# Kernel optimization log

Hardware: AMD Instinct MI355X
Metric: run time of the kernel (lower is better)

The kernel has to match this reference:

```python
import jax, jax.numpy as jnp
import numpy as np

N, E, D, H, O, G = 50000, 800000, 64, 64, 32, 64


def setup_inputs() -> dict:
    key = jax.random.key(0)
    ks = jax.random.split(key, 12)
    x = jax.random.normal(ks[0], (N, D), dtype=jnp.float32)
    edge_index = jax.random.randint(ks[1], (2, E), 0, N)
    batch = jnp.sort(jax.random.randint(ks[2], (N,), 0, G))

    def glorot(k, fan_in, fan_out):
        s = np.sqrt(6.0 / (fan_in + fan_out)).astype(np.float32)
        return jax.random.uniform(k, (fan_in, fan_out), jnp.float32, -s, s)

    return {
        "x": x,
        "edge_index": edge_index,
        "batch": batch,
        "W1": glorot(ks[3], D, H), "b1": jnp.zeros((H,), jnp.float32),
        "W2": glorot(ks[4], H, H), "b2": jnp.zeros((H,), jnp.float32),
        "W3": glorot(ks[5], H, H), "b3": jnp.zeros((H,), jnp.float32),
        "Wl": glorot(ks[6], H, O), "bl": jnp.zeros((O,), jnp.float32),
    }


def reference(x, edge_index, batch, W1, b1, W2, b2, W3, b3, Wl, bl):
    n = x.shape[0]
    # GCNConv default: add self-loops, symmetric deg^-1/2 normalization
    loop = jnp.arange(n, dtype=edge_index.dtype)
    src = jnp.concatenate([edge_index[0], loop])  # [E+N]
    dst = jnp.concatenate([edge_index[1], loop])
    deg = jax.ops.segment_sum(jnp.ones_like(src, dtype=x.dtype), dst, num_segments=n)
    dis = jax.lax.rsqrt(deg)  # deg >= 1 due to self-loops
    norm = (dis[src] * dis[dst])[:, None]  # [E+N, 1]

    def gcn(h, W, b):
        hw = h @ W                      # [N, H] small GEMM
        msg = hw[src] * norm            # gather + scale: [E+N, H]
        agg = jax.ops.segment_sum(msg, dst, num_segments=n)  # scatter-add
        return agg + b

    h = jax.nn.relu(gcn(x, W1, b1))
    h = jax.nn.relu(gcn(h, W2, b2))
    h = gcn(h, W3, b3)

    # global_mean_pool over graph ids
    counts = jax.ops.segment_sum(jnp.ones((n,), h.dtype), batch, num_segments=G)
    pooled = jax.ops.segment_sum(h, batch, num_segments=G) / counts[:, None]

    # dropout(p=0.5) is identity in eval mode
    return pooled @ Wl + bl
```

## Files before the change

### kernel.cpp

```cpp
#include <hip/hip_runtime.h>

#define HD 64
#define PSUB 16
#define NBLK 256
#define LOG_NBLK 8
#define NBKT 512

__device__ __forceinline__ unsigned short f2bf(float f) {
    union { float f; unsigned u; } v; v.f = f;
    unsigned r = v.u + 0x7FFF + ((v.u >> 16) & 1);
    return (unsigned short)(r >> 16);
}
__device__ __forceinline__ float u2f(unsigned u) {
    union { unsigned u; float f; } v; v.u = u;
    return v.f;
}


__global__ __launch_bounds__(256) void hist1_k(const int* __restrict__ dst,
                                               int* __restrict__ hist, int E, int chunk,
                                               float* __restrict__ partial, int psz)
{
    __shared__ int lh[NBKT];
    int t = threadIdx.x;
    for (int i = t; i < NBKT; i += 256) lh[i] = 0;
    for (int i = blockIdx.x * 256 + t; i < psz; i += gridDim.x * 256)
        partial[i] = 0.f;
    __syncthreads();
    int base = blockIdx.x * chunk;
    int end  = min(base + chunk, E);
    for (int i = base + t; i < end; i += 256)
        atomicAdd(&lh[dst[i] >> 7], 1);
    __syncthreads();
    for (int i = t; i < NBKT; i += 256)
        hist[blockIdx.x * NBKT + i] = lh[i];
}

__global__ __launch_bounds__(256) void scanA_k(const int* __restrict__ hist,
                                               int* __restrict__ tsum)
{
    __shared__ int s[256];
    int t = threadIdx.x;
    int l = blockIdx.x * 256 + t;
    int phys = (l & (NBLK - 1)) * NBKT + (l >> LOG_NBLK);
    s[t] = hist[phys];
    __syncthreads();
    for (int off = 128; off > 0; off >>= 1) {
        if (t < off) s[t] += s[t + off];
        __syncthreads();
    }
    if (t == 0) tsum[blockIdx.x] = s[0];
}

__global__ __launch_bounds__(1024) void scanB_k(int* __restrict__ tsum, int nb,
    const int* __restrict__ batch, int* __restrict__ gstart, int n, int G)
{
    __shared__ int s[1024];
    int t = threadIdx.x;
    int v = (t < nb) ? tsum[t] : 0;
    s[t] = v;
    __syncthreads();
    for (int off = 1; off < 1024; off <<= 1) {
        int u = (t >= off) ? s[t - off] : 0;
        __syncthreads();
        s[t] += u;
        __syncthreads();
    }
    if (t < nb) tsum[t] = s[t] - v;
    if (t <= G) {
        if (t == G) gstart[t] = n;
        else {
            int lo = 0, hi = n;
            while (lo < hi) { int m = (lo + hi) >> 1; if (batch[m] < t) lo = m + 1; else hi = m; }
            gstart[t] = lo;
        }
    }
}

__global__ __launch_bounds__(256) void scanC_k(const int* __restrict__ hist,
                                               const int* __restrict__ tsum,
                                               int* __restrict__ scanned)
{
    __shared__ int s[256];
    int t = threadIdx.x;
    int l = blockIdx.x * 256 + t;
    int phys = (l & (NBLK - 1)) * NBKT + (l >> LOG_NBLK);
    int own = hist[phys];
    s[t] = own;
    __syncthreads();
    for (int off = 1; off < 256; off <<= 1) {
        int u = (t >= off) ? s[t - off] : 0;
        __syncthreads();
        s[t] += u;
        __syncthreads();
    }
    scanned[l] = tsum[blockIdx.x] + s[t] - own;
}

__global__ __launch_bounds__(256) void append_k(const int* __restrict__ src,
    const int* __restrict__ dst, const int* __restrict__ scanned,
    int* __restrict__ pairs, int E, int chunk)
{
    __shared__ int cur[NBKT];
    int t = threadIdx.x;
    int blk = blockIdx.x;
    for (int i = t; i < NBKT; i += 256) cur[i] = scanned[i * NBLK + blk];
    __syncthreads();
    int base = blk * chunk;
    int end  = min(base + chunk, E);
    for (int i = base + t; i < end; i += 256) {
        int s = src[i], d = dst[i];
        int p = atomicAdd(&cur[d >> 7], 1);
        pairs[p] = (s << 7) | (d & 127);
    }
}

__global__ __launch_bounds__(256) void bucket_csr_k(const int* __restrict__ pairs,
    const int* __restrict__ scanned, int* __restrict__ offsets,
    float* __restrict__ dis, int* __restrict__ csr_src, int N, int E)
{
    __shared__ int cnt[128];
    __shared__ int sc[128];
    __shared__ int cur[128];
    int t = threadIdx.x;
    int b = blockIdx.x;
    int nodeBase = b * 128;
    int nNodes = min(128, N - nodeBase);
    int bBase = scanned[b * NBLK];
    int bEnd  = (b + 1 < NBKT) ? scanned[(b + 1) * NBLK] : E;

    if (t < 128) cnt[t] = 0;
    __syncthreads();
    for (int i = bBase + t; i < bEnd; i += 256)
        atomicAdd(&cnt[pairs[i] & 127], 1);
    __syncthreads();
    int myc = (t < 128) ? cnt[t] : 0;
    if (t < 128) sc[t] = myc;
    __syncthreads();
    for (int off = 1; off < 128; off <<= 1) {
        int u = (t < 128 && t >= off) ? sc[t - off] : 0;
        __syncthreads();
        if (t < 128) sc[t] += u;
        __syncthreads();
    }
    if (t < 128) {
        int excl = sc[t] - myc;
        cur[t] = excl;
        if (t < nNodes) {
            offsets[nodeBase + t] = bBase + excl;
            dis[nodeBase + t] = rsqrtf(1.0f + (float)myc);
        }
    }
    if (t == 0 && b == gridDim.x - 1) offsets[N] = E;
    __syncthreads();
    for (int i = bBase + t; i < bEnd; i += 256) {
        int pk = pairs[i];
        int pos = bBase + atomicAdd(&cur[pk & 127], 1);
        csr_src[pos] = ((unsigned)pk) >> 7;
    }
}


__global__ __launch_bounds__(256) void gemm64_k(
    const float* __restrict__ in, const float* __restrict__ W,
    const float* __restrict__ dis, unsigned short* __restrict__ outb, int n)
{
    __shared__ float HsT[HD][68];
    __shared__ float Ws[HD][HD];
    int t = threadIdx.x;
    int rowBase = blockIdx.x * 64;

    for (int i = t; i < HD * HD / 4; i += 256)
        ((float4*)Ws)[i] = ((const float4*)W)[i];

    if (blockIdx.x == 0 && t < 64)
        outb[(size_t)n * HD + t] = 0;

    {
        int k0 = (t & 15) * 4;
        for (int it = 0; it < 4; ++it) {
            int r = (t >> 4) + it * 16;
            int row = rowBase + r;
            float4 v = make_float4(0.f, 0.f, 0.f, 0.f);
            if (row < n)
                v = *(const float4*)&in[(size_t)row * HD + k0];
            HsT[k0 + 0][r] = v.x;
            HsT[k0 + 1][r] = v.y;
            HsT[k0 + 2][r] = v.z;
            HsT[k0 + 3][r] = v.w;
        }
    }
    __syncthreads();

    int c4 = (t & 15) * 4;
    int r4 = (t >> 4) * 4;
    float acc[4][4];
    #pragma unroll
    for (int i = 0; i < 4; ++i)
        #pragma unroll
        for (int j = 0; j < 4; ++j) acc[i][j] = 0.f;

    #pragma unroll 8
    for (int k = 0; k < HD; ++k) {
        float4 a = *(const float4*)&HsT[k][r4];
        float4 b = *(const float4*)&Ws[k][c4];
        acc[0][0] += a.x * b.x; acc[0][1] += a.x * b.y; acc[0][2] += a.x * b.z; acc[0][3] += a.x * b.w;
        acc[1][0] += a.y * b.x; acc[1][1] += a.y * b.y; acc[1][2] += a.y * b.z; acc[1][3] += a.y * b.w;
        acc[2][0] += a.z * b.x; acc[2][1] += a.z * b.y; acc[2][2] += a.z * b.z; acc[2][3] += a.z * b.w;
        acc[3][0] += a.w * b.x; acc[3][1] += a.w * b.y; acc[3][2] += a.w * b.z; acc[3][3] += a.w * b.w;
    }

    #pragma unroll
    for (int i = 0; i < 4; ++i) {
        int row = rowBase + r4 + i;
        if (row < n) {
            float ds = dis[row];
            ushort4 o;
            o.x = f2bf(ds * acc[i][0]); o.y = f2bf(ds * acc[i][1]);
            o.z = f2bf(ds * acc[i][2]); o.w = f2bf(ds * acc[i][3]);
            *(ushort4*)&outb[(size_t)row * HD + c4] = o;
        }
    }
}

__device__ __forceinline__ void gather4(const unsigned short* __restrict__ hwb,
    const int* __restrict__ offsets, const int* __restrict__ csr_src,
    int node, bool act, int n, int sub, int fl,
    float& a0, float& a1, float& a2, float& a3)
{
    int beg = 0, end = 0;
    if (act) { beg = offsets[node]; end = offsets[node + 1]; }
    int deg = end - beg;
    int md = deg;
    md = max(md, __shfl_xor(md, 16, 64));
    md = max(md, __shfl_xor(md, 32, 64));

    int nodeC = act ? node : n;
    uint2 sv = *(const uint2*)(hwb + ((size_t)nodeC << 6) + (fl << 2));
    a0 = u2f(sv.x << 16); a1 = u2f(sv.x & 0xFFFF0000u);
    a2 = u2f(sv.y << 16); a3 = u2f(sv.y & 0xFFFF0000u);

    int base = sub << 4;
    int idxv = (fl < deg) ? csr_src[beg + fl] : n;
    for (int jb = 0; jb < md; jb += 16) {
        int e2 = jb + 16 + fl;
        int nidx = (e2 < deg) ? csr_src[beg + e2] : n;
        {
            uint2 g[8];
            #pragma unroll
            for (int j = 0; j < 8; ++j) {
                int row = __shfl(idxv, base + j, 64);
                g[j] = *(const uint2*)(hwb + ((size_t)row << 6) + (fl << 2));
            }
            #pragma unroll
            for (int j = 0; j < 8; ++j) {
                a0 += u2f(g[j].x << 16); a1 += u2f(g[j].x & 0xFFFF0000u);
                a2 += u2f(g[j].y << 16); a3 += u2f(g[j].y & 0xFFFF0000u);
            }
        }
        if (jb + 8 < md) {
            uint2 g[8];
            #pragma unroll
            for (int j = 0; j < 8; ++j) {
                int row = __shfl(idxv, base + 8 + j, 64);
                g[j] = *(const uint2*)(hwb + ((size_t)row << 6) + (fl << 2));
            }
            #pragma unroll
            for (int j = 0; j < 8; ++j) {
                a0 += u2f(g[j].x << 16); a1 += u2f(g[j].x & 0xFFFF0000u);
                a2 += u2f(g[j].y << 16); a3 += u2f(g[j].y & 0xFFFF0000u);
            }
        }
        idxv = nidx;
    }
}

__global__ __launch_bounds__(256) void agg_gemm_k(
    const unsigned short* __restrict__ hwb, const float* __restrict__ dis,
    const int* __restrict__ offsets, const int* __restrict__ csr_src,
    const float* __restrict__ b_prev, const float* __restrict__ W,
    unsigned short* __restrict__ outb, int n)
{
    __shared__ float As[16][68];
    __shared__ float Ws[HD][HD];
    int t    = threadIdx.x;
    int lane = t & 63;
    int sub  = lane >> 4;
    int fl   = lane & 15;
    int w    = t >> 6;
    int nib  = w * 4 + sub;
    int nodeBase = blockIdx.x * 16;
    int node = nodeBase + nib;
    bool act = node < n;

    for (int i = t; i < HD * HD / 4; i += 256)
        ((float4*)Ws)[i] = ((const float4*)W)[i];

    if (blockIdx.x == 0 && t < 64)
        outb[(size_t)n * HD + t] = 0;

    float a0, a1, a2, a3;
    gather4(hwb, offsets, csr_src, node, act, n, sub, fl, a0, a1, a2, a3);

    float ds = act ? dis[node] : 0.f;
    int c0 = fl << 2;
    float4 bb = *(const float4*)&b_prev[c0];
    float4 v;
    v.x = fmaxf(a0 * ds + bb.x, 0.f);
    v.y = fmaxf(a1 * ds + bb.y, 0.f);
    v.z = fmaxf(a2 * ds + bb.z, 0.f);
    v.w = fmaxf(a3 * ds + bb.w, 0.f);
    *(float4*)&As[nib][c0] = v;
    __syncthreads();

    int r  = t & 15;
    int c4 = (t >> 4) << 2;
    float acc0 = 0.f, acc1 = 0.f, acc2 = 0.f, acc3 = 0.f;
    #pragma unroll 4
    for (int k = 0; k < HD; k += 4) {
        float4 a  = *(const float4*)&As[r][k];
        float4 w0 = *(const float4*)&Ws[k + 0][c4];
        float4 w1 = *(const float4*)&Ws[k + 1][c4];
        float4 w2 = *(const float4*)&Ws[k + 2][c4];
        float4 w3 = *(const float4*)&Ws[k + 3][c4];
        acc0 += a.x * w0.x + a.y * w1.x + a.z * w2.x + a.w * w3.x;
        acc1 += a.x * w0.y + a.y * w1.y + a.z * w2.y + a.w * w3.y;
        acc2 += a.x * w0.z + a.y * w1.z + a.z * w2.z + a.w * w3.z;
        acc3 += a.x * w0.w + a.y * w1.w + a.z * w2.w + a.w * w3.w;
    }
    int orow = nodeBase + r;
    if (orow < n) {
        float d2 = dis[orow];
        ushort4 o;
        o.x = f2bf(d2 * acc0); o.y = f2bf(d2 * acc1);
        o.z = f2bf(d2 * acc2); o.w = f2bf(d2 * acc3);
        *(ushort4*)&outb[(size_t)orow * HD + c4] = o;
    }
}

__global__ __launch_bounds__(256) void agg_pool4_k(const unsigned short* __restrict__ hwb,
    const float* __restrict__ dis, const int* __restrict__ offsets,
    const int* __restrict__ csr_src, const int* __restrict__ batch,
    float* __restrict__ partial, int n)
{
    __shared__ float sh[16][68];
    __shared__ int gids[16];
    __shared__ int allsame;
    int t    = threadIdx.x;
    int lane = t & 63;
    int sub  = lane >> 4;
    int fl   = lane & 15;
    int w    = t >> 6;
    int nib  = w * 4 + sub;
    int node = blockIdx.x * 16 + nib;
    bool act = node < n;

    float a0, a1, a2, a3;
    gather4(hwb, offsets, csr_src, node, act, n, sub, fl, a0, a1, a2, a3);

    float ds = act ? dis[node] : 0.f;
    *(float4*)&sh[nib][fl << 2] = make_float4(a0 * ds, a1 * ds, a2 * ds, a3 * ds);
    if (fl == 0) gids[nib] = act ? batch[node] : -1;
    __syncthreads();

    if (t == 0) {
        int g0 = gids[0];
        int ok = (g0 >= 0);
        #pragma unroll
        for (int r = 1; r < 16; ++r) ok &= (gids[r] == g0);
        allsame = ok;
    }
    __syncthreads();

    int slot = blockIdx.x & (PSUB - 1);
    if (allsame) {
        if (t < 64) {
            float s = 0.f;
            #pragma unroll
            for (int r = 0; r < 16; ++r) s += sh[r][t];
            atomicAdd(&partial[((size_t)gids[0] * PSUB + slot) * HD + t], s);
        }
    } else {
        int c  = t & 63;
        int r0 = w * 4;
        int ga = gids[r0], gb = gids[r0 + 1], gc = gids[r0 + 2], gd = gids[r0 + 3];
        if (ga == gb && gb == gc && gc == gd && ga >= 0) {
            float v = sh[r0][c] + sh[r0 + 1][c] + sh[r0 + 2][c] + sh[r0 + 3][c];
            atomicAdd(&partial[((size_t)ga * PSUB + slot) * HD + c], v);
        } else {
            if (ga >= 0) atomicAdd(&partial[((size_t)ga * PSUB + slot) * HD + c], sh[r0][c]);
            if (gb >= 0) atomicAdd(&partial[((size_t)gb * PSUB + slot) * HD + c], sh[r0 + 1][c]);
            if (gc >= 0) atomicAdd(&partial[((size_t)gc * PSUB + slot) * HD + c], sh[r0 + 2][c]);
            if (gd >= 0) atomicAdd(&partial[((size_t)gd * PSUB + slot) * HD + c], sh[r0 + 3][c]);
        }
    }
}

__global__ __launch_bounds__(64) void pool2_k(const float* __restrict__ partial,
    const int* __restrict__ gstart, const float* __restrict__ b3,
    const float* __restrict__ Wl, const float* __restrict__ bl,
    float* __restrict__ out, int O)
{
    __shared__ float pooled[HD];
    int g = blockIdx.x;
    int t = threadIdx.x;
    float sum = 0.0f;
    #pragma unroll
    for (int s = 0; s < PSUB; ++s)
        sum += partial[((size_t)g * PSUB + s) * HD + t];
    float cnt = (float)(gstart[g + 1] - gstart[g]);
    pooled[t] = sum / cnt + b3[t];
    __syncthreads();
    if (t < O) {
        float acc = bl[t];
        #pragma unroll
        for (int k = 0; k < HD; ++k) acc += pooled[k] * Wl[k * O + t];
        out[g * O + t] = acc;
    }
}

extern "C" void kernel_launch(void* const* d_in, const int* in_sizes, int n_in,
                              void* d_out, int out_size, void* d_ws, size_t ws_size,
                              hipStream_t stream)
{
    const float* x    = (const float*)d_in[0];
    const int*   ei   = (const int*)d_in[1];
    const int*   batch= (const int*)d_in[2];
    const float* W1   = (const float*)d_in[3];
    const float* b1   = (const float*)d_in[4];
    const float* W2   = (const float*)d_in[5];
    const float* b2   = (const float*)d_in[6];
    const float* W3   = (const float*)d_in[7];
    const float* b3   = (const float*)d_in[8];
    const float* Wl   = (const float*)d_in[9];
    const float* bl   = (const float*)d_in[10];
    float* out = (float*)d_out;

    const int N = in_sizes[0] / HD;
    const int E = in_sizes[1] / 2;
    const int O = in_sizes[10];
    const int G = out_size / O;

    const int* src = ei;
    const int* dst = ei + E;

    char* p = (char*)d_ws;
    auto take = [&](size_t bytes) { char* r = p; p += (bytes + 255) & ~(size_t)255; return r; };
    int*   csr_src = (int*)  take((size_t)(E + 256) * 4);
    int*   offsets = (int*)  take((size_t)(N + 1) * 4);
    float* dis     = (float*)take((size_t)N * 4);
    int*   gstart  = (int*)  take((size_t)(G + 1) * 4);
    float* partial = (float*)take((size_t)G * PSUB * HD * 4);
    unsigned short* hwb  = (unsigned short*)take((size_t)(N + 1) * HD * 2);
    unsigned short* hwb2 = (unsigned short*)take((size_t)(N + 1) * HD * 2);

    int* pairs   = (int*)hwb;
    int* hist    = (int*)hwb2;
    int* scanned = hist + NBLK * NBKT;
    int* tsum    = scanned + NBLK * NBKT;

    const int TB = 256;
    int chunk   = (E + NBLK - 1) / NBLK;
    int ntiles  = (NBLK * NBKT) / 256;
    int nb_gemm = (N + 63) / 64;
    int nb_agg4 = (N + 15) / 16;
    int nbuck   = (N + 127) / 128;
    int psz     = G * PSUB * HD;

    hist1_k<<<NBLK, TB, 0, stream>>>(dst, hist, E, chunk, partial, psz);
    scanA_k<<<ntiles, TB, 0, stream>>>(hist, tsum);
    scanB_k<<<1, 1024, 0, stream>>>(tsum, ntiles, batch, gstart, N, G);
    scanC_k<<<ntiles, TB, 0, stream>>>(hist, tsum, scanned);
    append_k<<<NBLK, TB, 0, stream>>>(src, dst, scanned, pairs, E, chunk);
    bucket_csr_k<<<nbuck, TB, 0, stream>>>(pairs, scanned, offsets, dis, csr_src, N, E);

    gemm64_k<<<nb_gemm, TB, 0, stream>>>(x, W1, dis, hwb, N);

    agg_gemm_k<<<nb_agg4, TB, 0, stream>>>(hwb, dis, offsets, csr_src, b1, W2, hwb2, N);

    agg_gemm_k<<<nb_agg4, TB, 0, stream>>>(hwb2, dis, offsets, csr_src, b2, W3, hwb, N);

    agg_pool4_k<<<nb_agg4, TB, 0, stream>>>(hwb, dis, offsets, csr_src, batch, partial, N);

    pool2_k<<<G, 64, 0, stream>>>(partial, gstart, b3, Wl, bl, out, O);
}
```

Baseline: 193.3 us.

## Fold three-kernel histogram scan into append kernel with redundant per-block scans

Removes the separate scanA/scanB/scanC kernels. Each append block now recomputes its own per-bucket offsets by summing the transposed histogram rows and doing a block-wide scan over bucket totals, and block 0 publishes the bucket bases. The graph-start binary search moves into the histogram kernel. This cuts three kernel launches and their serialization, at the cost of every append block redundantly reading the full 512x256 histogram.

```diff
diff --git a/kernel.cpp b/kernel.cpp
--- a/kernel.cpp
+++ b/kernel.cpp
@@ -3,7 +3,6 @@
 #define HD 64
 #define PSUB 16
 #define NBLK 256
-#define LOG_NBLK 8
 #define NBKT 512
 
 __device__ __forceinline__ unsigned short f2bf(float f) {
@@ -18,56 +17,16 @@
 
 
 __global__ __launch_bounds__(256) void hist1_k(const int* __restrict__ dst,
-                                               int* __restrict__ hist, int E, int chunk,
-                                               float* __restrict__ partial, int psz)
+    int* __restrict__ hist, int E, int chunk,
+    float* __restrict__ partial, int psz,
+    const int* __restrict__ batch, int* __restrict__ gstart, int n, int G)
 {
     __shared__ int lh[NBKT];
     int t = threadIdx.x;
     for (int i = t; i < NBKT; i += 256) lh[i] = 0;
     for (int i = blockIdx.x * 256 + t; i < psz; i += gridDim.x * 256)
         partial[i] = 0.f;
-    __syncthreads();
-    int base = blockIdx.x * chunk;
-    int end  = min(base + chunk, E);
-    for (int i = base + t; i < end; i += 256)
-        atomicAdd(&lh[dst[i] >> 7], 1);
-    __syncthreads();
-    for (int i = t; i < NBKT; i += 256)
-        hist[blockIdx.x * NBKT + i] = lh[i];
-}
-
-__global__ __launch_bounds__(256) void scanA_k(const int* __restrict__ hist,
-                                               int* __restrict__ tsum)
-{
-    __shared__ int s[256];
-    int t = threadIdx.x;
-    int l = blockIdx.x * 256 + t;
-    int phys = (l & (NBLK - 1)) * NBKT + (l >> LOG_NBLK);
-    s[t] = hist[phys];
-    __syncthreads();
-    for (int off = 128; off > 0; off >>= 1) {
-        if (t < off) s[t] += s[t + off];
-        __syncthreads();
-    }
-    if (t == 0) tsum[blockIdx.x] = s[0];
-}
-
-__global__ __launch_bounds__(1024) void scanB_k(int* __restrict__ tsum, int nb,
-    const int* __restrict__ batch, int* __restrict__ gstart, int n, int G)
-{
-    __shared__ int s[1024];
-    int t = threadIdx.x;
-    int v = (t < nb) ? tsum[t] : 0;
-    s[t] = v;
-    __syncthreads();
-    for (int off = 1; off < 1024; off <<= 1) {
-        int u = (t >= off) ? s[t - off] : 0;
-        __syncthreads();
-        s[t] += u;
-        __syncthreads();
-    }
-    if (t < nb) tsum[t] = s[t] - v;
-    if (t <= G) {
+    if (blockIdx.x == 0 && t <= G) {
         if (t == G) gstart[t] = n;
         else {
             int lo = 0, hi = n;
@@ -75,38 +34,64 @@
             gstart[t] = lo;
         }
     }
-}
-
-__global__ __launch_bounds__(256) void scanC_k(const int* __restrict__ hist,
-                                               const int* __restrict__ tsum,
-                                               int* __restrict__ scanned)
-{
-    __shared__ int s[256];
+    __syncthreads();
+    int base = blockIdx.x * chunk;
+    int end  = min(base + chunk, E);
+    for (int i = base + t; i < end; i += 256)
+        atomicAdd(&lh[dst[i] >> 7], 1);
+    __syncthreads();
+    for (int i = t; i < NBKT; i += 256)
+        hist[i * NBLK + blockIdx.x] = lh[i];
+}
+
+__global__ __launch_bounds__(256) void append2_k(const int* __restrict__ src,
+    const int* __restrict__ dst, const int* __restrict__ hist,
+    int* __restrict__ pairs, int* __restrict__ bucketb, int E, int chunk)
+{
+    __shared__ int cur[NBKT];
+    __shared__ int tot[NBKT];
+    __shared__ int ps[256];
     int t = threadIdx.x;
-    int l = blockIdx.x * 256 + t;
-    int phys = (l & (NBLK - 1)) * NBKT + (l >> LOG_NBLK);
-    int own = hist[phys];
-    s[t] = own;
+    int k = blockIdx.x;
+
+    for (int b = t; b < NBKT; b += 256) {
+        const int4* row4 = (const int4*)(hist + b * NBLK);
+        int below = 0, total = 0;
+        #pragma unroll 4
+        for (int c = 0; c < NBLK / 4; ++c) {
+            int4 h = row4[c];
+            int k0 = c * 4;
+            total += h.x + h.y + h.z + h.w;
+            below += ((k0 + 0) < k ? h.x : 0) + ((k0 + 1) < k ? h.y : 0)
+                   + ((k0 + 2) < k ? h.z : 0) + ((k0 + 3) < k ? h.w : 0);
+        }
+        tot[b] = total;
+        cur[b] = below;
+    }
+    __syncthreads();
+
+    int pa = tot[2 * t], pb = tot[2 * t + 1];
+    ps[t] = pa + pb;
     __syncthreads();
     for (int off = 1; off < 256; off <<= 1) {
-        int u = (t >= off) ? s[t - off] : 0;
+        int u = (t >= off) ? ps[t - off] : 0;
         __syncthreads();
-        s[t] += u;
+        ps[t] += u;
         __syncthreads();
     }
-    scanned[l] = tsum[blockIdx.x] + s[t] - own;
-}
-
-__global__ __launch_bounds__(256) void append_k(const int* __restrict__ src,
-    const int* __restrict__ dst, const int* __restrict__ scanned,
-    int* __restrict__ pairs, int E, int chunk)
-{
-    __shared__ int cur[NBKT];
-    int t = threadIdx.x;
-    int blk = blockIdx.x;
-    for (int i = t; i < NBKT; i += 256) cur[i] = scanned[i * NBLK + blk];
-    __syncthreads();
-    int base = blk * chunk;
+    int excl  = ps[t] - (pa + pb);
+    int base0 = excl;
+    int base1 = excl + pa;
+    cur[2 * t]     += base0;
+    cur[2 * t + 1] += base1;
+    if (k == 0) {
+        bucketb[2 * t]     = base0;
+        bucketb[2 * t + 1] = base1;
+        if (t == 0) bucketb[NBKT] = E;
+    }
+    __syncthreads();
+
+    int base = k * chunk;
     int end  = min(base + chunk, E);
     for (int i = base + t; i < end; i += 256) {
         int s = src[i], d = dst[i];
@@ -116,7 +101,7 @@
 }
 
 __global__ __launch_bounds__(256) void bucket_csr_k(const int* __restrict__ pairs,
-    const int* __restrict__ scanned, int* __restrict__ offsets,
+    const int* __restrict__ bucketb, int* __restrict__ offsets,
     float* __restrict__ dis, int* __restrict__ csr_src, int N, int E)
 {
     __shared__ int cnt[128];
@@ -126,8 +111,8 @@
     int b = blockIdx.x;
     int nodeBase = b * 128;
     int nNodes = min(128, N - nodeBase);
-    int bBase = scanned[b * NBLK];
-    int bEnd  = (b + 1 < NBKT) ? scanned[(b + 1) * NBLK] : E;
+    int bBase = bucketb[b];
+    int bEnd  = bucketb[b + 1];
 
     if (t < 128) cnt[t] = 0;
     __syncthreads();
@@ -456,23 +441,19 @@
 
     int* pairs   = (int*)hwb;
     int* hist    = (int*)hwb2;
-    int* scanned = hist + NBLK * NBKT;
-    int* tsum    = scanned + NBLK * NBKT;
+    int* bucketb = hist + NBKT * NBLK;
 
     const int TB = 256;
     int chunk   = (E + NBLK - 1) / NBLK;
-    int ntiles  = (NBLK * NBKT) / 256;
     int nb_gemm = (N + 63) / 64;
     int nb_agg4 = (N + 15) / 16;
     int nbuck   = (N + 127) / 128;
     int psz     = G * PSUB * HD;
 
-    hist1_k<<<NBLK, TB, 0, stream>>>(dst, hist, E, chunk, partial, psz);
-    scanA_k<<<ntiles, TB, 0, stream>>>(hist, tsum);
-    scanB_k<<<1, 1024, 0, stream>>>(tsum, ntiles, batch, gstart, N, G);
-    scanC_k<<<ntiles, TB, 0, stream>>>(hist, tsum, scanned);
-    append_k<<<NBLK, TB, 0, stream>>>(src, dst, scanned, pairs, E, chunk);
-    bucket_csr_k<<<nbuck, TB, 0, stream>>>(pairs, scanned, offsets, dis, csr_src, N, E);
+    hist1_k<<<NBLK, TB, 0, stream>>>(dst, hist, E, chunk, partial, psz,
+                                     batch, gstart, N, G);
+    append2_k<<<NBLK, TB, 0, stream>>>(src, dst, hist, pairs, bucketb, E, chunk);
+    bucket_csr_k<<<nbuck, TB, 0, stream>>>(pairs, bucketb, offsets, dis, csr_src, N, E);
 
     gemm64_k<<<nb_gemm, TB, 0, stream>>>(x, W1, dis, hwb, N);
 
```

Result: slower. 197.4 us (+2.1%).

## Assign 8 lanes per node with 16-byte gathers in aggregation kernels

Applied to the files above, without the earlier changes.

The gather is remapped from 16 lanes per node reading 8 bytes each to 8 lanes per node reading 16 bytes each, so each wave handles 8 nodes and each block 32 nodes. The fused aggregate+GEMM and aggregate+pool kernels are resized to match: a 32-row shared tile, 8 output columns per thread, and pooling checks over 8-node groups. The aim is fewer, wider memory transactions and more nodes in flight per wave, which amortizes the per-row index shuffles. In exchange each thread needs more registers and the per-wave max-degree loop now spans 8 nodes, which can increase divergence.

```diff
diff --git a/kernel.cpp b/kernel.cpp
--- a/kernel.cpp
+++ b/kernel.cpp
@@ -223,53 +223,42 @@
     }
 }
 
-__device__ __forceinline__ void gather4(const unsigned short* __restrict__ hwb,
+__device__ __forceinline__ void gather8(const unsigned short* __restrict__ hwb,
     const int* __restrict__ offsets, const int* __restrict__ csr_src,
-    int node, bool act, int n, int sub, int fl,
-    float& a0, float& a1, float& a2, float& a3)
+    int node, bool act, int n, int fl, float* a )
 {
     int beg = 0, end = 0;
     if (act) { beg = offsets[node]; end = offsets[node + 1]; }
     int deg = end - beg;
     int md = deg;
+    md = max(md, __shfl_xor(md, 8, 64));
     md = max(md, __shfl_xor(md, 16, 64));
     md = max(md, __shfl_xor(md, 32, 64));
 
     int nodeC = act ? node : n;
-    uint2 sv = *(const uint2*)(hwb + ((size_t)nodeC << 6) + (fl << 2));
-    a0 = u2f(sv.x << 16); a1 = u2f(sv.x & 0xFFFF0000u);
-    a2 = u2f(sv.y << 16); a3 = u2f(sv.y & 0xFFFF0000u);
-
-    int base = sub << 4;
+    uint4 sv = *(const uint4*)(hwb + ((size_t)nodeC << 6) + (fl << 3));
+    a[0] = u2f(sv.x << 16); a[1] = u2f(sv.x & 0xFFFF0000u);
+    a[2] = u2f(sv.y << 16); a[3] = u2f(sv.y & 0xFFFF0000u);
+    a[4] = u2f(sv.z << 16); a[5] = u2f(sv.z & 0xFFFF0000u);
+    a[6] = u2f(sv.w << 16); a[7] = u2f(sv.w & 0xFFFF0000u);
+
+    int grpbase = threadIdx.x & 56;
     int idxv = (fl < deg) ? csr_src[beg + fl] : n;
-    for (int jb = 0; jb < md; jb += 16) {
-        int e2 = jb + 16 + fl;
+    for (int jb = 0; jb < md; jb += 8) {
+        int e2 = jb + 8 + fl;
         int nidx = (e2 < deg) ? csr_src[beg + e2] : n;
-        {
-            uint2 g[8];
-            #pragma unroll
-            for (int j = 0; j < 8; ++j) {
-                int row = __shfl(idxv, base + j, 64);
-                g[j] = *(const uint2*)(hwb + ((size_t)row << 6) + (fl << 2));
-            }
-            #pragma unroll
-            for (int j = 0; j < 8; ++j) {
-                a0 += u2f(g[j].x << 16); a1 += u2f(g[j].x & 0xFFFF0000u);
-                a2 += u2f(g[j].y << 16); a3 += u2f(g[j].y & 0xFFFF0000u);
-            }
-        }
-        if (jb + 8 < md) {
-            uint2 g[8];
-            #pragma unroll
-            for (int j = 0; j < 8; ++j) {
-                int row = __shfl(idxv, base + 8 + j, 64);
-                g[j] = *(const uint2*)(hwb + ((size_t)row << 6) + (fl << 2));
-            }
-            #pragma unroll
-            for (int j = 0; j < 8; ++j) {
-                a0 += u2f(g[j].x << 16); a1 += u2f(g[j].x & 0xFFFF0000u);
-                a2 += u2f(g[j].y << 16); a3 += u2f(g[j].y & 0xFFFF0000u);
-            }
+        uint4 g[8];
+        #pragma unroll
+        for (int j = 0; j < 8; ++j) {
+            int row = __shfl(idxv, grpbase + j, 64);
+            g[j] = *(const uint4*)(hwb + ((size_t)row << 6) + (fl << 3));
+        }
+        #pragma unroll
+        for (int j = 0; j < 8; ++j) {
+            a[0] += u2f(g[j].x << 16); a[1] += u2f(g[j].x & 0xFFFF0000u);
+            a[2] += u2f(g[j].y << 16); a[3] += u2f(g[j].y & 0xFFFF0000u);
+            a[4] += u2f(g[j].z << 16); a[5] += u2f(g[j].z & 0xFFFF0000u);
+            a[6] += u2f(g[j].w << 16); a[7] += u2f(g[j].w & 0xFFFF0000u);
         }
         idxv = nidx;
     }
@@ -281,15 +270,15 @@
     const float* __restrict__ b_prev, const float* __restrict__ W,
     unsigned short* __restrict__ outb, int n)
 {
-    __shared__ float As[16][68];
+    __shared__ float As[32][68];
     __shared__ float Ws[HD][HD];
     int t    = threadIdx.x;
     int lane = t & 63;
-    int sub  = lane >> 4;
-    int fl   = lane & 15;
+    int grp  = lane >> 3;
+    int fl   = lane & 7;
     int w    = t >> 6;
-    int nib  = w * 4 + sub;
-    int nodeBase = blockIdx.x * 16;
+    int nib  = w * 8 + grp;
+    int nodeBase = blockIdx.x * 32;
     int node = nodeBase + nib;
     bool act = node < n;
 
@@ -299,67 +288,72 @@
     if (blockIdx.x == 0 && t < 64)
         outb[(size_t)n * HD + t] = 0;
 
-    float a0, a1, a2, a3;
-    gather4(hwb, offsets, csr_src, node, act, n, sub, fl, a0, a1, a2, a3);
+    float a[8];
+    gather8(hwb, offsets, csr_src, node, act, n, fl, a);
 
     float ds = act ? dis[node] : 0.f;
-    int c0 = fl << 2;
-    float4 bb = *(const float4*)&b_prev[c0];
-    float4 v;
-    v.x = fmaxf(a0 * ds + bb.x, 0.f);
-    v.y = fmaxf(a1 * ds + bb.y, 0.f);
-    v.z = fmaxf(a2 * ds + bb.z, 0.f);
-    v.w = fmaxf(a3 * ds + bb.w, 0.f);
-    *(float4*)&As[nib][c0] = v;
-    __syncthreads();
-
-    int r  = t & 15;
-    int c4 = (t >> 4) << 2;
-    float acc0 = 0.f, acc1 = 0.f, acc2 = 0.f, acc3 = 0.f;
+    int c0 = fl << 3;
+    float4 b0 = *(const float4*)&b_prev[c0];
+    float4 b1 = *(const float4*)&b_prev[c0 + 4];
+    float4 v0, v1;
+    v0.x = fmaxf(a[0] * ds + b0.x, 0.f); v0.y = fmaxf(a[1] * ds + b0.y, 0.f);
+    v0.z = fmaxf(a[2] * ds + b0.z, 0.f); v0.w = fmaxf(a[3] * ds + b0.w, 0.f);
+    v1.x = fmaxf(a[4] * ds + b1.x, 0.f); v1.y = fmaxf(a[5] * ds + b1.y, 0.f);
+    v1.z = fmaxf(a[6] * ds + b1.z, 0.f); v1.w = fmaxf(a[7] * ds + b1.w, 0.f);
+    *(float4*)&As[nib][c0]     = v0;
+    *(float4*)&As[nib][c0 + 4] = v1;
+    __syncthreads();
+
+    int r  = t & 31;
+    int c8 = (t >> 5) << 3;
+    float s0 = 0.f, s1 = 0.f, s2 = 0.f, s3 = 0.f, s4 = 0.f, s5 = 0.f, s6 = 0.f, s7 = 0.f;
     #pragma unroll 4
     for (int k = 0; k < HD; k += 4) {
-        float4 a  = *(const float4*)&As[r][k];
-        float4 w0 = *(const float4*)&Ws[k + 0][c4];
-        float4 w1 = *(const float4*)&Ws[k + 1][c4];
-        float4 w2 = *(const float4*)&Ws[k + 2][c4];
-        float4 w3 = *(const float4*)&Ws[k + 3][c4];
-        acc0 += a.x * w0.x + a.y * w1.x + a.z * w2.x + a.w * w3.x;
-        acc1 += a.x * w0.y + a.y * w1.y + a.z * w2.y + a.w * w3.y;
-        acc2 += a.x * w0.z + a.y * w1.z + a.z * w2.z + a.w * w3.z;
-        acc3 += a.x * w0.w + a.y * w1.w + a.z * w2.w + a.w * w3.w;
+        float4 aa = *(const float4*)&As[r][k];
+        #pragma unroll
+        for (int kk = 0; kk < 4; ++kk) {
+            float av = (kk == 0) ? aa.x : (kk == 1) ? aa.y : (kk == 2) ? aa.z : aa.w;
+            float4 w0 = *(const float4*)&Ws[k + kk][c8];
+            float4 w1 = *(const float4*)&Ws[k + kk][c8 + 4];
+            s0 += av * w0.x; s1 += av * w0.y; s2 += av * w0.z; s3 += av * w0.w;
+            s4 += av * w1.x; s5 += av * w1.y; s6 += av * w1.z; s7 += av * w1.w;
+        }
     }
     int orow = nodeBase + r;
     if (orow < n) {
         float d2 = dis[orow];
-        ushort4 o;
-        o.x = f2bf(d2 * acc0); o.y = f2bf(d2 * acc1);
-        o.z = f2bf(d2 * acc2); o.w = f2bf(d2 * acc3);
-        *(ushort4*)&outb[(size_t)orow * HD + c4] = o;
-    }
-}
-
-__global__ __launch_bounds__(256) void agg_pool4_k(const unsigned short* __restrict__ hwb,
+        ushort4 o0, o1;
+        o0.x = f2bf(d2 * s0); o0.y = f2bf(d2 * s1); o0.z = f2bf(d2 * s2); o0.w = f2bf(d2 * s3);
+        o1.x = f2bf(d2 * s4); o1.y = f2bf(d2 * s5); o1.z = f2bf(d2 * s6); o1.w = f2bf(d2 * s7);
+        *(ushort4*)&outb[(size_t)orow * HD + c8]     = o0;
+        *(ushort4*)&outb[(size_t)orow * HD + c8 + 4] = o1;
+    }
+}
+
+__global__ __launch_bounds__(256) void agg_pool8_k(const unsigned short* __restrict__ hwb,
     const float* __restrict__ dis, const int* __restrict__ offsets,
     const int* __restrict__ csr_src, const int* __restrict__ batch,
     float* __restrict__ partial, int n)
 {
-    __shared__ float sh[16][68];
-    __shared__ int gids[16];
+    __shared__ float sh[32][68];
+    __shared__ int gids[32];
     __shared__ int allsame;
     int t    = threadIdx.x;
     int lane = t & 63;
-    int sub  = lane >> 4;
-    int fl   = lane & 15;
+    int grp  = lane >> 3;
+    int fl   = lane & 7;
     int w    = t >> 6;
-    int nib  = w * 4 + sub;
-    int node = blockIdx.x * 16 + nib;
+    int nib  = w * 8 + grp;
+    int node = blockIdx.x * 32 + nib;
     bool act = node < n;
 
-    float a0, a1, a2, a3;
-    gather4(hwb, offsets, csr_src, node, act, n, sub, fl, a0, a1, a2, a3);
+    float a[8];
+    gather8(hwb, offsets, csr_src, node, act, n, fl, a);
 
     float ds = act ? dis[node] : 0.f;
-    *(float4*)&sh[nib][fl << 2] = make_float4(a0 * ds, a1 * ds, a2 * ds, a3 * ds);
+    int c0 = fl << 3;
+    *(float4*)&sh[nib][c0]     = make_float4(a[0] * ds, a[1] * ds, a[2] * ds, a[3] * ds);
+    *(float4*)&sh[nib][c0 + 4] = make_float4(a[4] * ds, a[5] * ds, a[6] * ds, a[7] * ds);
     if (fl == 0) gids[nib] = act ? batch[node] : -1;
     __syncthreads();
 
@@ -367,7 +361,7 @@
         int g0 = gids[0];
         int ok = (g0 >= 0);
         #pragma unroll
-        for (int r = 1; r < 16; ++r) ok &= (gids[r] == g0);
+        for (int r = 1; r < 32; ++r) ok &= (gids[r] == g0);
         allsame = ok;
     }
     __syncthreads();
@@ -377,21 +371,28 @@
         if (t < 64) {
             float s = 0.f;
             #pragma unroll
-            for (int r = 0; r < 16; ++r) s += sh[r][t];
+            for (int r = 0; r < 32; ++r) s += sh[r][t];
             atomicAdd(&partial[((size_t)gids[0] * PSUB + slot) * HD + t], s);
         }
     } else {
-        int c  = t & 63;
-        int r0 = w * 4;
-        int ga = gids[r0], gb = gids[r0 + 1], gc = gids[r0 + 2], gd = gids[r0 + 3];
-        if (ga == gb && gb == gc && gc == gd && ga >= 0) {
-            float v = sh[r0][c] + sh[r0 + 1][c] + sh[r0 + 2][c] + sh[r0 + 3][c];
-            atomicAdd(&partial[((size_t)ga * PSUB + slot) * HD + c], v);
+        int c  = lane;
+        int r0 = w * 8;
+        int gw = gids[r0];
+        bool same8 = (gw >= 0);
+        #pragma unroll
+        for (int rr = 1; rr < 8; ++rr) same8 &= (gids[r0 + rr] == gw);
+        if (same8) {
+            float v = 0.f;
+            #pragma unroll
+            for (int rr = 0; rr < 8; ++rr) v += sh[r0 + rr][c];
+            atomicAdd(&partial[((size_t)gw * PSUB + slot) * HD + c], v);
         } else {
-            if (ga >= 0) atomicAdd(&partial[((size_t)ga * PSUB + slot) * HD + c], sh[r0][c]);
-            if (gb >= 0) atomicAdd(&partial[((size_t)gb * PSUB + slot) * HD + c], sh[r0 + 1][c]);
-            if (gc >= 0) atomicAdd(&partial[((size_t)gc * PSUB + slot) * HD + c], sh[r0 + 2][c]);
-            if (gd >= 0) atomicAdd(&partial[((size_t)gd * PSUB + slot) * HD + c], sh[r0 + 3][c]);
+            #pragma unroll
+            for (int rr = 0; rr < 8; ++rr) {
+                int gg = gids[r0 + rr];
+                if (gg >= 0)
+                    atomicAdd(&partial[((size_t)gg * PSUB + slot) * HD + c], sh[r0 + rr][c]);
+            }
         }
     }
 }
@@ -463,7 +464,7 @@
     int chunk   = (E + NBLK - 1) / NBLK;
     int ntiles  = (NBLK * NBKT) / 256;
     int nb_gemm = (N + 63) / 64;
-    int nb_agg4 = (N + 15) / 16;
+    int nb_agg8 = (N + 31) / 32;
     int nbuck   = (N + 127) / 128;
     int psz     = G * PSUB * HD;
 
@@ -476,11 +477,11 @@
 
     gemm64_k<<<nb_gemm, TB, 0, stream>>>(x, W1, dis, hwb, N);
 
-    agg_gemm_k<<<nb_agg4, TB, 0, stream>>>(hwb, dis, offsets, csr_src, b1, W2, hwb2, N);
-
-    agg_gemm_k<<<nb_agg4, TB, 0, stream>>>(hwb2, dis, offsets, csr_src, b2, W3, hwb, N);
-
-    agg_pool4_k<<<nb_agg4, TB, 0, stream>>>(hwb, dis, offsets, csr_src, batch, partial, N);
+    agg_gemm_k<<<nb_agg8, TB, 0, stream>>>(hwb, dis, offsets, csr_src, b1, W2, hwb2, N);
+
+    agg_gemm_k<<<nb_agg8, TB, 0, stream>>>(hwb2, dis, offsets, csr_src, b2, W3, hwb, N);
+
+    agg_pool8_k<<<nb_agg8, TB, 0, stream>>>(hwb, dis, offsets, csr_src, batch, partial, N);
 
     pool2_k<<<G, 64, 0, stream>>>(partial, gstart, b3, Wl, bl, out, O);
 }
```

After: 184.9 us (median of 2 runs). 4.4% less time.
